# Kernel tuning notes

Measured on AMD Instinct MI355X. Metric: run time of the kernel, lower is better.

The kernel has to match this reference:

```python
import jax, jax.numpy as jnp
import numpy as np

N = 65536      # H*W pixels (256x256)
S = 1024       # superpixels
C = 128        # input channels
HIDE = 128     # hidden width
OUT = 64       # per-branch width (hide//2, concat=True)
CLS = 16       # classes
E_A = 16384    # superpixel adjacency edges
E_IMP = 6144   # importance (k=6) edges
E_PX = 1048576 # pixel row/col mask edges
EPS = 1e-5


def setup_inputs() -> dict:
    key = jax.random.key(0)
    ks = iter(jax.random.split(key, 64))
    nrm = lambda shape: jax.random.normal(next(ks), shape, dtype=jnp.float32) * 0.05
    uni = lambda shape, lo=0.0, hi=1.0: jax.random.uniform(next(ks), shape, dtype=jnp.float32, minval=lo, maxval=hi)
    ridx = lambda shape, hi: jax.random.randint(next(ks), shape, 0, hi, dtype=jnp.int32)
    d = {}
    d['x'] = jax.random.normal(next(ks), (N, C), dtype=jnp.float32)
    d['Q'] = uni((N, S))
    d['prelin_w'] = nrm((C, HIDE)); d['prelin_b'] = jnp.zeros((HIDE,), jnp.float32)
    d['bn0_g'] = jnp.ones((HIDE,), jnp.float32); d['bn0_b'] = jnp.zeros((HIDE,), jnp.float32)
    d['bn0_m'] = nrm((HIDE,)); d['bn0_v'] = uni((HIDE,), 0.5, 1.5)
    d['mmpn_w'] = nrm((5, HIDE, HIDE)); d['mmpn_b'] = jnp.zeros((5, HIDE), jnp.float32)
    d['mmpn_bn_g'] = jnp.ones((5, HIDE), jnp.float32); d['mmpn_bn_b'] = jnp.zeros((5, HIDE), jnp.float32)
    d['mmpn_bn_m'] = nrm((5, HIDE)); d['mmpn_bn_v'] = uni((5, HIDE), 0.5, 1.5)
    d['A_val'] = uni((E_A,)); d['imp_val'] = uni((E_IMP,))
    d['px_rowv_w'] = nrm((2, HIDE, OUT)); d['px_rowv_b'] = jnp.zeros((2, OUT), jnp.float32)
    d['px_colv_w'] = nrm((2, HIDE, OUT)); d['px_colv_b'] = jnp.zeros((2, OUT), jnp.float32)
    d['px_rowq_w'] = nrm((2, HIDE, OUT)); d['px_rowq_b'] = jnp.zeros((2, OUT), jnp.float32)
    d['px_colq_w'] = nrm((2, HIDE, OUT)); d['px_colq_b'] = jnp.zeros((2, OUT), jnp.float32)
    d['px_bn_g'] = jnp.ones((2, HIDE), jnp.float32); d['px_bn_b'] = jnp.zeros((2, HIDE), jnp.float32)
    d['px_bn_m'] = nrm((2, HIDE)); d['px_bn_v'] = uni((2, HIDE), 0.5, 1.5)
    d['final_w'] = nrm((HIDE, CLS)); d['final_b'] = jnp.zeros((CLS,), jnp.float32)
    d['A_src'] = ridx((E_A,), S); d['A_dst'] = ridx((E_A,), S)
    d['imp_src'] = ridx((E_IMP,), S); d['imp_dst'] = ridx((E_IMP,), S)
    d['row_src'] = ridx((E_PX,), N); d['row_dst'] = ridx((E_PX,), N)
    d['col_src'] = ridx((E_PX,), N); d['col_dst'] = ridx((E_PX,), N)
    return d


def _bn(x, g, b, m, v):
    # BatchNorm1d, eval mode (running stats)
    return g * (x - m) * jax.lax.rsqrt(v + EPS) + b


def _lrelu(x):
    return jnp.where(x >= 0, x, 0.01 * x)


def _ln(x):
    # F.layer_norm without affine params
    mu = jnp.mean(x, axis=-1, keepdims=True)
    var = jnp.mean(jnp.square(x - mu), axis=-1, keepdims=True)
    return (x - mu) * jax.lax.rsqrt(var + EPS)


def _seg_softmax(scores, ids, n):
    m = jax.ops.segment_max(scores, ids, num_segments=n)
    e = jnp.exp(scores - m[ids])
    d = jax.ops.segment_sum(e, ids, num_segments=n)
    return e / d[ids]


def _forward(x, Q, prelin_w, prelin_b, bn0_g, bn0_b, bn0_m, bn0_v,
             mmpn_w, mmpn_b, mmpn_bn_g, mmpn_bn_b, mmpn_bn_m, mmpn_bn_v,
             A_val, imp_val,
             px_rowv_w, px_rowv_b, px_colv_w, px_colv_b,
             px_rowq_w, px_rowq_b, px_colq_w, px_colq_b,
             px_bn_g, px_bn_b, px_bn_m, px_bn_v,
             final_w, final_b,
             A_src, A_dst, imp_src, imp_dst, row_src, row_dst, col_src, col_dst):
    x0 = _bn(x @ prelin_w + prelin_b, bn0_g, bn0_b, bn0_m, bn0_v)  # [N, HIDE]

    # ---- Hyperpixel_MMPN branch ----
    ncQ = Q / jnp.sum(Q, axis=0, keepdims=True)       # column-normalized Q
    hp = ncQ.T @ x0                                    # [S, HIDE]
    for i in range(5):
        h = hp @ mmpn_w[i] + mmpn_b[i]
        agg = jax.ops.segment_sum(A_val[:, None] * h[A_src], A_dst, num_segments=S)
        agg = agg + jax.ops.segment_sum(imp_val[:, None] * hp[imp_src], imp_dst, num_segments=S)
        hp = _lrelu(_bn(agg, mmpn_bn_g[i], mmpn_bn_b[i], mmpn_bn_m[i], mmpn_bn_v[i]))
    hyp = Q @ hp                                       # [N, HIDE]

    # ---- Pixel sparse-former branch ----
    px = x0
    for j in range(2):
        rowv = px @ px_rowv_w[j] + px_rowv_b[j]        # [N, OUT]
        colv = px @ px_colv_w[j] + px_colv_b[j]
        rowQ = _ln(px @ px_rowq_w[j] + px_rowq_b[j])
        colQ = _ln(px @ px_colq_w[j] + px_colq_b[j])
        rs = jnp.sum(rowQ[row_src] * rowQ[row_dst], axis=1) / OUT
        cs = jnp.sum(colQ[col_src] * colQ[col_dst], axis=1) / OUT
        ra = _seg_softmax(rs, row_src, N)
        ca = _seg_softmax(cs, col_src, N)
        rowout = jax.ops.segment_sum(rowv[row_dst] * ra[:, None], row_src, num_segments=N)
        colout = jax.ops.segment_sum(colv[col_dst] * ca[:, None], col_src, num_segments=N)
        out = jnp.concatenate((rowout, colout), axis=1)  # [N, HIDE]
        px = _lrelu(_bn(out, px_bn_g[j], px_bn_b[j], px_bn_m[j], px_bn_v[j]))

    H1 = hyp + px
    return jax.nn.softmax(H1 @ final_w + final_b, axis=-1)


def reference(x, Q, prelin_w, prelin_b, bn0_g, bn0_b, bn0_m, bn0_v,
              mmpn_w, mmpn_b, mmpn_bn_g, mmpn_bn_b, mmpn_bn_m, mmpn_bn_v,
              A_val, imp_val,
              px_rowv_w, px_rowv_b, px_colv_w, px_colv_b,
              px_rowq_w, px_rowq_b, px_colq_w, px_colq_b,
              px_bn_g, px_bn_b, px_bn_m, px_bn_v,
              final_w, final_b,
              A_src, A_dst, imp_src, imp_dst, row_src, row_dst, col_src, col_dst):
    return _forward(x, Q, prelin_w, prelin_b, bn0_g, bn0_b, bn0_m, bn0_v,
                    mmpn_w, mmpn_b, mmpn_bn_g, mmpn_bn_b, mmpn_bn_m, mmpn_bn_v,
                    A_val, imp_val,
                    px_rowv_w, px_rowv_b, px_colv_w, px_colv_b,
                    px_rowq_w, px_rowq_b, px_colq_w, px_colq_b,
                    px_bn_g, px_bn_b, px_bn_m, px_bn_v,
                    final_w, final_b,
                    A_src, A_dst, imp_src, imp_dst, row_src, row_dst, col_src, col_dst)
```

## Files before the change

kernel.cpp:

```cpp
#include <hip/hip_runtime.h>
#include <math.h>

#define N_PIX 65536
#define S_SP  1024
#define C_IN  128
#define HIDE  128
#define OUTW  64
#define NCLS  16
#define E_A   16384
#define E_IMP 6144
#define E_PX  1048576
#define EPSV  1e-5f

typedef __attribute__((ext_vector_type(4))) float f32x4;
typedef __attribute__((ext_vector_type(8))) short bf16x8;

__device__ inline ushort f2bf(float f) {
  uint u = __builtin_bit_cast(uint, f);
  uint r = (u + 0x7FFFu + ((u >> 16) & 1u)) >> 16;
  return (ushort)r;
}

__global__ __launch_bounds__(256) void k_x0(
    const float* __restrict__ x, const float* __restrict__ W,
    const float* __restrict__ bias, const float* __restrict__ g,
    const float* __restrict__ bb, const float* __restrict__ m,
    const float* __restrict__ vv, float* __restrict__ out) {
  __shared__ float Wl[128 * 128];
  __shared__ float Xl[32 * 128];
  int t = threadIdx.x;
  int n0 = blockIdx.x * 32;
  {
    const float4* Wg = (const float4*)W;
    float4* Wd = (float4*)Wl;
#pragma unroll
    for (int i = 0; i < 16; ++i) Wd[t + 256 * i] = Wg[t + 256 * i];
    const float4* Xg = (const float4*)(x + (size_t)n0 * 128);
    float4* Xd = (float4*)Xl;
#pragma unroll
    for (int i = 0; i < 4; ++i) Xd[t + 256 * i] = Xg[t + 256 * i];
  }
  __syncthreads();
  int ht = t & 31, nt = t >> 5;
  int h0 = ht * 4, r0 = nt * 4;
  float acc[4][4];
#pragma unroll
  for (int c = 0; c < 4; ++c) {
    float bv = bias[h0 + c];
#pragma unroll
    for (int r = 0; r < 4; ++r) acc[r][c] = bv;
  }
  for (int k = 0; k < 128; k += 4) {
    float4 xr[4], wk[4];
#pragma unroll
    for (int r = 0; r < 4; ++r) xr[r] = *(const float4*)&Xl[(r0 + r) * 128 + k];
#pragma unroll
    for (int kk = 0; kk < 4; ++kk) wk[kk] = *(const float4*)&Wl[(k + kk) * 128 + h0];
#pragma unroll
    for (int r = 0; r < 4; ++r) {
      float xs[4] = {xr[r].x, xr[r].y, xr[r].z, xr[r].w};
#pragma unroll
      for (int kk = 0; kk < 4; ++kk) {
        acc[r][0] += xs[kk] * wk[kk].x;
        acc[r][1] += xs[kk] * wk[kk].y;
        acc[r][2] += xs[kk] * wk[kk].z;
        acc[r][3] += xs[kk] * wk[kk].w;
      }
    }
  }
#pragma unroll
  for (int c = 0; c < 4; ++c) {
    int h = h0 + c;
    float sc = g[h] * rsqrtf(vv[h] + EPSV);
    float mb = m[h], bo = bb[h];
#pragma unroll
    for (int r = 0; r < 4; ++r) acc[r][c] = sc * (acc[r][c] - mb) + bo;
  }
#pragma unroll
  for (int r = 0; r < 4; ++r) {
    *(float4*)&out[(size_t)(n0 + r0 + r) * 128 + h0] =
        make_float4(acc[r][0], acc[r][1], acc[r][2], acc[r][3]);
  }
}

__global__ __launch_bounds__(256) void k_cast(
    const float* __restrict__ Q, ushort* __restrict__ Qt,
    float* __restrict__ csum, ushort* __restrict__ Qbf) {
  __shared__ ushort Ot[64 * 258];
  __shared__ float Cs[64];
  int t = threadIdx.x;
  int nt = blockIdx.x & 255, st = blockIdx.x >> 8;
  int n0 = nt * 256, s0 = st * 64;
  int lr = t & 15, lg = t >> 4;
  if (t < 64) Cs[t] = 0.f;
  __syncthreads();
  float sums[4] = {0.f, 0.f, 0.f, 0.f};
#pragma unroll
  for (int nb = 0; nb < 4; ++nb) {
    ushort hh[4][4];
#pragma unroll
    for (int u = 0; u < 4; ++u) {
      int n = n0 + nb * 64 + lg * 4 + u;
      float4 q = *(const float4*)&Q[(size_t)n * 1024 + s0 + lr * 4];
      sums[0] += q.x; sums[1] += q.y; sums[2] += q.z; sums[3] += q.w;
      hh[u][0] = f2bf(q.x); hh[u][1] = f2bf(q.y);
      hh[u][2] = f2bf(q.z); hh[u][3] = f2bf(q.w);
      if (Qbf) {
        uint2 w;
        w.x = (uint)hh[u][0] | ((uint)hh[u][1] << 16);
        w.y = (uint)hh[u][2] | ((uint)hh[u][3] << 16);
        *(uint2*)&Qbf[(size_t)n * 1024 + s0 + lr * 4] = w;
      }
    }
#pragma unroll
    for (int v = 0; v < 4; ++v) {
      uint lo = (uint)hh[0][v] | ((uint)hh[1][v] << 16);
      uint hi = (uint)hh[2][v] | ((uint)hh[3][v] << 16);
      ushort* p = &Ot[(lr * 4 + v) * 258 + nb * 64 + lg * 4];
      *(uint*)p = lo;
      *(uint*)(p + 2) = hi;
    }
  }
#pragma unroll
  for (int v = 0; v < 4; ++v) atomicAdd(&Cs[lr * 4 + v], sums[v]);
  __syncthreads();
  if (t < 64) atomicAdd(&csum[s0 + t], Cs[t]);
#pragma unroll
  for (int i = 0; i < 16; ++i) {
    int v2 = i * 256 + t;
    int s_loc = v2 >> 6, nq = v2 & 63;
    const ushort* p = &Ot[s_loc * 258 + nq * 4];
    uint2 o;
    o.x = *(const uint*)p;
    o.y = *(const uint*)(p + 2);
    *(uint2*)&Qt[(size_t)(s0 + s_loc) * 65536 + n0 + nq * 4] = o;
  }
}

__global__ __launch_bounds__(256) void k_xT(
    const float* __restrict__ x0, ushort* __restrict__ x0T) {
  __shared__ ushort Ot[128 * 258];
  int t = threadIdx.x;
  int n0 = blockIdx.x * 256;
  int lr = t & 31, lg = t >> 5;
#pragma unroll
  for (int nb = 0; nb < 8; ++nb) {
    ushort hh[4][4];
#pragma unroll
    for (int u = 0; u < 4; ++u) {
      int n = n0 + nb * 32 + lg * 4 + u;
      float4 q = *(const float4*)&x0[(size_t)n * 128 + lr * 4];
      hh[u][0] = f2bf(q.x); hh[u][1] = f2bf(q.y);
      hh[u][2] = f2bf(q.z); hh[u][3] = f2bf(q.w);
    }
#pragma unroll
    for (int v = 0; v < 4; ++v) {
      uint lo = (uint)hh[0][v] | ((uint)hh[1][v] << 16);
      uint hi = (uint)hh[2][v] | ((uint)hh[3][v] << 16);
      ushort* p = &Ot[(lr * 4 + v) * 258 + nb * 32 + lg * 4];
      *(uint*)p = lo;
      *(uint*)(p + 2) = hi;
    }
  }
  __syncthreads();
#pragma unroll
  for (int i = 0; i < 32; ++i) {
    int v2 = i * 256 + t;
    int h = v2 >> 6, nq = v2 & 63;
    const ushort* p = &Ot[h * 258 + nq * 4];
    uint2 o;
    o.x = *(const uint*)p;
    o.y = *(const uint*)(p + 2);
    *(uint2*)&x0T[(size_t)h * 65536 + n0 + nq * 4] = o;
  }
}

__global__ __launch_bounds__(256) void k_hpT(
    const float* __restrict__ hp, ushort* __restrict__ hpT) {
  __shared__ ushort Ot[128 * 258];
  int t = threadIdx.x;
  int s0 = blockIdx.x * 256;
  int lr = t & 31, lg = t >> 5;
#pragma unroll
  for (int sb = 0; sb < 8; ++sb) {
    ushort hh[4][4];
#pragma unroll
    for (int u = 0; u < 4; ++u) {
      int s = s0 + sb * 32 + lg * 4 + u;
      float4 q = *(const float4*)&hp[(size_t)s * 128 + lr * 4];
      hh[u][0] = f2bf(q.x); hh[u][1] = f2bf(q.y);
      hh[u][2] = f2bf(q.z); hh[u][3] = f2bf(q.w);
    }
#pragma unroll
    for (int v = 0; v < 4; ++v) {
      uint lo = (uint)hh[0][v] | ((uint)hh[1][v] << 16);
      uint hi = (uint)hh[2][v] | ((uint)hh[3][v] << 16);
      ushort* p = &Ot[(lr * 4 + v) * 258 + sb * 32 + lg * 4];
      *(uint*)p = lo;
      *(uint*)(p + 2) = hi;
    }
  }
  __syncthreads();
#pragma unroll
  for (int i = 0; i < 32; ++i) {
    int v2 = i * 256 + t;
    int h = v2 >> 6, sq = v2 & 63;
    const ushort* p = &Ot[h * 258 + sq * 4];
    uint2 o;
    o.x = *(const uint*)p;
    o.y = *(const uint*)(p + 2);
    *(uint2*)&hpT[(size_t)h * 1024 + s0 + sq * 4] = o;
  }
}

__device__ __forceinline__ void mfma_tile128(const ushort* Al, const ushort* Bl,
                                             f32x4 acc[4][4], int wr, int wc,
                                             int lr, int lq) {
#pragma unroll
  for (int kh = 0; kh < 2; ++kh) {
    bf16x8 af[4], bf[4];
#pragma unroll
    for (int i = 0; i < 4; ++i)
      af[i] = *(const bf16x8*)&Al[(wr * 64 + i * 16 + lr) * 72 + kh * 32 + lq * 8];
#pragma unroll
    for (int j = 0; j < 4; ++j)
      bf[j] = *(const bf16x8*)&Bl[(wc * 64 + j * 16 + lr) * 72 + kh * 32 + lq * 8];
#pragma unroll
    for (int i = 0; i < 4; ++i)
#pragma unroll
      for (int j = 0; j < 4; ++j)
        acc[i][j] = __builtin_amdgcn_mfma_f32_16x16x32_bf16(af[i], bf[j],
                                                            acc[i][j], 0, 0, 0);
  }
}

__global__ __launch_bounds__(256) void k_hpu2(
    const ushort* __restrict__ Qt, const ushort* __restrict__ x0T,
    float* __restrict__ hp_part) {
  __shared__ ushort Al[2][128 * 72];
  __shared__ ushort Bl[2][128 * 72];
  int t = threadIdx.x;
  int st = blockIdx.x & 7, kb = blockIdx.x >> 3;
  int s0 = st * 128;
  int wv = t >> 6, lane = t & 63;
  int wr = wv >> 1, wc = wv & 1;
  int lr = lane & 15, lq = lane >> 4;
  int sr = t >> 3, sg = t & 7;
  const ushort* Ab = Qt + (size_t)(s0 + sr) * 65536 + (size_t)kb * 1024 + sg * 8;
  const ushort* Bb = x0T + (size_t)sr * 65536 + (size_t)kb * 1024 + sg * 8;
  f32x4 acc[4][4];
#pragma unroll
  for (int i = 0; i < 4; ++i)
#pragma unroll
    for (int j = 0; j < 4; ++j) acc[i][j] = (f32x4){0.f, 0.f, 0.f, 0.f};
  uint4 ra[4], rb[4];
#pragma unroll
  for (int i = 0; i < 4; ++i) {
    ra[i] = *(const uint4*)(Ab + (size_t)i * 32 * 65536);
    rb[i] = *(const uint4*)(Bb + (size_t)i * 32 * 65536);
  }
#pragma unroll
  for (int i = 0; i < 4; ++i) {
    *(uint4*)&Al[0][(sr + 32 * i) * 72 + sg * 8] = ra[i];
    *(uint4*)&Bl[0][(sr + 32 * i) * 72 + sg * 8] = rb[i];
  }
  __syncthreads();
  for (int c = 0; c < 16; ++c) {
    int p = c & 1;
    if (c < 15) {
      int ko = (c + 1) * 64;
#pragma unroll
      for (int i = 0; i < 4; ++i) {
        ra[i] = *(const uint4*)(Ab + (size_t)i * 32 * 65536 + ko);
        rb[i] = *(const uint4*)(Bb + (size_t)i * 32 * 65536 + ko);
      }
    }
    mfma_tile128(Al[p], Bl[p], acc, wr, wc, lr, lq);
    if (c < 15) {
      int q = p ^ 1;
#pragma unroll
      for (int i = 0; i < 4; ++i) {
        *(uint4*)&Al[q][(sr + 32 * i) * 72 + sg * 8] = ra[i];
        *(uint4*)&Bl[q][(sr + 32 * i) * 72 + sg * 8] = rb[i];
      }
    }
    __syncthreads();
  }
  float* outp = hp_part + (size_t)kb * 131072;
#pragma unroll
  for (int i = 0; i < 4; ++i) {
    int s_g = s0 + wr * 64 + i * 16 + lq * 4;
#pragma unroll
    for (int j = 0; j < 4; ++j) {
      int h = wc * 64 + j * 16 + lr;
#pragma unroll
      for (int r = 0; r < 4; ++r)
        outp[(size_t)(s_g + r) * 128 + h] = acc[i][j][r];
    }
  }
}

__global__ void k_hpred(const float* __restrict__ part,
                        const float* __restrict__ csum, float* __restrict__ hp) {
  int tid = blockIdx.x * 256 + threadIdx.x;
  float s = 0.f;
  for (int kb = 0; kb < 64; ++kb) s += part[(size_t)kb * 131072 + tid];
  hp[tid] = s / csum[tid >> 7];
}

__global__ __launch_bounds__(256) void k_hyp_bf(
    const ushort* __restrict__ Qbf, const ushort* __restrict__ hpT,
    float* __restrict__ hyp) {
  __shared__ ushort Al[2][128 * 72];
  __shared__ ushort Bl[2][128 * 72];
  int t = threadIdx.x;
  int n0 = blockIdx.x * 128;
  int wv = t >> 6, lane = t & 63;
  int wr = wv >> 1, wc = wv & 1;
  int lr = lane & 15, lq = lane >> 4;
  int sr = t >> 3, sg = t & 7;
  const ushort* Ab = Qbf + (size_t)(n0 + sr) * 1024 + sg * 8;
  const ushort* Bb = hpT + (size_t)sr * 1024 + sg * 8;
  f32x4 acc[4][4];
#pragma unroll
  for (int i = 0; i < 4; ++i)
#pragma unroll
    for (int j = 0; j < 4; ++j) acc[i][j] = (f32x4){0.f, 0.f, 0.f, 0.f};
  uint4 ra[4], rb[4];
#pragma unroll
  for (int i = 0; i < 4; ++i) {
    ra[i] = *(const uint4*)(Ab + (size_t)i * 32 * 1024);
    rb[i] = *(const uint4*)(Bb + (size_t)i * 32 * 1024);
  }
#pragma unroll
  for (int i = 0; i < 4; ++i) {
    *(uint4*)&Al[0][(sr + 32 * i) * 72 + sg * 8] = ra[i];
    *(uint4*)&Bl[0][(sr + 32 * i) * 72 + sg * 8] = rb[i];
  }
  __syncthreads();
  for (int c = 0; c < 16; ++c) {
    int p = c & 1;
    if (c < 15) {
      int ko = (c + 1) * 64;
#pragma unroll
      for (int i = 0; i < 4; ++i) {
        ra[i] = *(const uint4*)(Ab + (size_t)i * 32 * 1024 + ko);
        rb[i] = *(const uint4*)(Bb + (size_t)i * 32 * 1024 + ko);
      }
    }
    mfma_tile128(Al[p], Bl[p], acc, wr, wc, lr, lq);
    if (c < 15) {
      int q = p ^ 1;
#pragma unroll
      for (int i = 0; i < 4; ++i) {
        *(uint4*)&Al[q][(sr + 32 * i) * 72 + sg * 8] = ra[i];
        *(uint4*)&Bl[q][(sr + 32 * i) * 72 + sg * 8] = rb[i];
      }
    }
    __syncthreads();
  }
#pragma unroll
  for (int i = 0; i < 4; ++i) {
    int n_g = n0 + wr * 64 + i * 16 + lq * 4;
#pragma unroll
    for (int j = 0; j < 4; ++j) {
      int h = wc * 64 + j * 16 + lr;
#pragma unroll
      for (int r = 0; r < 4; ++r)
        hyp[(size_t)(n_g + r) * 128 + h] = acc[i][j][r];
    }
  }
}

__global__ __launch_bounds__(256) void k_hyp_f32(
    const float* __restrict__ Q, const ushort* __restrict__ hpT,
    float* __restrict__ hyp) {
  __shared__ ushort Al[2][128 * 72];
  __shared__ ushort Bl[2][128 * 72];
  int t = threadIdx.x;
  int n0 = blockIdx.x * 128;
  int wv = t >> 6, lane = t & 63;
  int wr = wv >> 1, wc = wv & 1;
  int lr = lane & 15, lq = lane >> 4;
  int ar = t >> 4, ag = t & 15;
  int sr = t >> 3, sg = t & 7;
  const float* Af = Q + (size_t)(n0 + ar) * 1024 + ag * 4;
  const ushort* Bb = hpT + (size_t)sr * 1024 + sg * 8;
  f32x4 acc[4][4];
#pragma unroll
  for (int i = 0; i < 4; ++i)
#pragma unroll
    for (int j = 0; j < 4; ++j) acc[i][j] = (f32x4){0.f, 0.f, 0.f, 0.f};
  float4 rf[8];
  uint4 rb[4];
#pragma unroll
  for (int i = 0; i < 8; ++i) rf[i] = *(const float4*)(Af + (size_t)i * 16 * 1024);
#pragma unroll
  for (int i = 0; i < 4; ++i) rb[i] = *(const uint4*)(Bb + (size_t)i * 32 * 1024);
#pragma unroll
  for (int i = 0; i < 8; ++i) {
    uint2 pk;
    pk.x = (uint)f2bf(rf[i].x) | ((uint)f2bf(rf[i].y) << 16);
    pk.y = (uint)f2bf(rf[i].z) | ((uint)f2bf(rf[i].w) << 16);
    *(uint2*)&Al[0][(ar + 16 * i) * 72 + ag * 4] = pk;
  }
#pragma unroll
  for (int i = 0; i < 4; ++i)
    *(uint4*)&Bl[0][(sr + 32 * i) * 72 + sg * 8] = rb[i];
  __syncthreads();
  for (int c = 0; c < 16; ++c) {
    int p = c & 1;
    if (c < 15) {
      int ko = (c + 1) * 64;
#pragma unroll
      for (int i = 0; i < 8; ++i)
        rf[i] = *(const float4*)(Af + (size_t)i * 16 * 1024 + ko);
#pragma unroll
      for (int i = 0; i < 4; ++i)
        rb[i] = *(const uint4*)(Bb + (size_t)i * 32 * 1024 + ko);
    }
    mfma_tile128(Al[p], Bl[p], acc, wr, wc, lr, lq);
    if (c < 15) {
      int q = p ^ 1;
#pragma unroll
      for (int i = 0; i < 8; ++i) {
        uint2 pk;
        pk.x = (uint)f2bf(rf[i].x) | ((uint)f2bf(rf[i].y) << 16);
        pk.y = (uint)f2bf(rf[i].z) | ((uint)f2bf(rf[i].w) << 16);
        *(uint2*)&Al[q][(ar + 16 * i) * 72 + ag * 4] = pk;
      }
#pragma unroll
      for (int i = 0; i < 4; ++i)
        *(uint4*)&Bl[q][(sr + 32 * i) * 72 + sg * 8] = rb[i];
    }
    __syncthreads();
  }
#pragma unroll
  for (int i = 0; i < 4; ++i) {
    int n_g = n0 + wr * 64 + i * 16 + lq * 4;
#pragma unroll
    for (int j = 0; j < 4; ++j) {
      int h = wc * 64 + j * 16 + lr;
#pragma unroll
      for (int r = 0; r < 4; ++r)
        hyp[(size_t)(n_g + r) * 128 + h] = acc[i][j][r];
    }
  }
}

__global__ __launch_bounds__(256) void k_slin(
    const float* __restrict__ A, const float* __restrict__ W,
    const float* __restrict__ bias, float* __restrict__ out) {
  __shared__ float Wl[128 * 128];
  __shared__ float Xl[32 * 128];
  int t = threadIdx.x;
  int n0 = blockIdx.x * 32;
  {
    const float4* Wg = (const float4*)W;
    float4* Wd = (float4*)Wl;
#pragma unroll
    for (int i = 0; i < 16; ++i) Wd[t + 256 * i] = Wg[t + 256 * i];
    const float4* Xg = (const float4*)(A + (size_t)n0 * 128);
    float4* Xd = (float4*)Xl;
#pragma unroll
    for (int i = 0; i < 4; ++i) Xd[t + 256 * i] = Xg[t + 256 * i];
  }
  __syncthreads();
  int ht = t & 31, nt = t >> 5;
  int h0 = ht * 4, r0 = nt * 4;
  float acc[4][4];
#pragma unroll
  for (int c = 0; c < 4; ++c) {
    float bv = bias[h0 + c];
#pragma unroll
    for (int r = 0; r < 4; ++r) acc[r][c] = bv;
  }
  for (int k = 0; k < 128; k += 4) {
    float4 xr[4], wk[4];
#pragma unroll
    for (int r = 0; r < 4; ++r) xr[r] = *(const float4*)&Xl[(r0 + r) * 128 + k];
#pragma unroll
    for (int kk = 0; kk < 4; ++kk) wk[kk] = *(const float4*)&Wl[(k + kk) * 128 + h0];
#pragma unroll
    for (int r = 0; r < 4; ++r) {
      float xs[4] = {xr[r].x, xr[r].y, xr[r].z, xr[r].w};
#pragma unroll
      for (int kk = 0; kk < 4; ++kk) {
        acc[r][0] += xs[kk] * wk[kk].x;
        acc[r][1] += xs[kk] * wk[kk].y;
        acc[r][2] += xs[kk] * wk[kk].z;
        acc[r][3] += xs[kk] * wk[kk].w;
      }
    }
  }
#pragma unroll
  for (int r = 0; r < 4; ++r) {
    *(float4*)&out[(size_t)(n0 + r0 + r) * 128 + h0] =
        make_float4(acc[r][0], acc[r][1], acc[r][2], acc[r][3]);
  }
}

__global__ void k_edge_mmpn(
    const float* __restrict__ htmp, const float* __restrict__ hp,
    const float* __restrict__ A_val, const int* __restrict__ A_src,
    const int* __restrict__ A_dst, const float* __restrict__ imp_val,
    const int* __restrict__ imp_src, const int* __restrict__ imp_dst,
    float* __restrict__ agg) {
  long tid = (long)blockIdx.x * 256 + threadIdx.x;
  if (tid < (long)E_A * HIDE) {
    int e = (int)(tid >> 7), h = (int)(tid & 127);
    atomicAdd(&agg[(size_t)A_dst[e] * HIDE + h],
              A_val[e] * htmp[(size_t)A_src[e] * HIDE + h]);
  } else {
    long t2 = tid - (long)E_A * HIDE;
    if (t2 < (long)E_IMP * HIDE) {
      int e = (int)(t2 >> 7), h = (int)(t2 & 127);
      atomicAdd(&agg[(size_t)imp_dst[e] * HIDE + h],
                imp_val[e] * hp[(size_t)imp_src[e] * HIDE + h]);
    }
  }
}

__global__ void k_mmpn_bn(const float* __restrict__ agg, const float* __restrict__ g,
                          const float* __restrict__ b, const float* __restrict__ m,
                          const float* __restrict__ v, float* __restrict__ hp) {
  int tid = blockIdx.x * 256 + threadIdx.x;
  int h = tid & 127;
  float sc = g[h] * rsqrtf(v[h] + EPSV);
  float y = sc * (agg[tid] - m[h]) + b[h];
  hp[tid] = y >= 0.f ? y : 0.01f * y;
}

__global__ __launch_bounds__(256) void k_pxlin(
    const float* __restrict__ px, const float* __restrict__ Wrv,
    const float* __restrict__ Wcv, const float* __restrict__ Wrq,
    const float* __restrict__ Wcq, const float* __restrict__ brv,
    const float* __restrict__ bcv, const float* __restrict__ brq,
    const float* __restrict__ bcq, float* __restrict__ out) {
  __shared__ float Xl[32 * 128];
  __shared__ float Wl[32 * 256];
  int t = threadIdx.x;
  int n0 = blockIdx.x * 32;
  {
    float4* Xd = (float4*)Xl;
    const float4* Xg = (const float4*)(px + (size_t)n0 * 128);
#pragma unroll
    for (int it = 0; it < 4; ++it) Xd[t + 256 * it] = Xg[t + 256 * it];
  }
  int ct = t & 63, nt = t >> 6;
  int c0 = ct * 4, r0 = nt * 8;
  float acc[8][4];
  {
    int mt = c0 >> 6, cb = c0 & 63;
    const float* bs = mt == 0 ? brv : mt == 1 ? bcv : mt == 2 ? brq : bcq;
#pragma unroll
    for (int c = 0; c < 4; ++c) {
      float bv = bs[cb + c];
#pragma unroll
      for (int r = 0; r < 8; ++r) acc[r][c] = bv;
    }
  }
  for (int kc = 0; kc < 4; ++kc) {
    int k0 = kc * 32;
    __syncthreads();
    {
#pragma unroll
      for (int it = 0; it < 8; ++it) {
        int v = t + 256 * it;
        int kk = v >> 6, cq = v & 63;
        int c = cq * 4;
        int mt = c >> 6, cb = c & 63;
        const float* Ws = mt == 0 ? Wrv : mt == 1 ? Wcv : mt == 2 ? Wrq : Wcq;
        *(float4*)&Wl[kk * 256 + c] = *(const float4*)&Ws[(size_t)(k0 + kk) * 64 + cb];
      }
    }
    __syncthreads();
    for (int k = 0; k < 32; k += 4) {
      float4 wq[4];
#pragma unroll
      for (int kk = 0; kk < 4; ++kk) wq[kk] = *(const float4*)&Wl[(k + kk) * 256 + c0];
#pragma unroll
      for (int r = 0; r < 8; ++r) {
        float4 xq = *(const float4*)&Xl[(r0 + r) * 128 + k0 + k];
        float xs[4] = {xq.x, xq.y, xq.z, xq.w};
#pragma unroll
        for (int kk = 0; kk < 4; ++kk) {
          acc[r][0] += xs[kk] * wq[kk].x;
          acc[r][1] += xs[kk] * wq[kk].y;
          acc[r][2] += xs[kk] * wq[kk].z;
          acc[r][3] += xs[kk] * wq[kk].w;
        }
      }
    }
  }
#pragma unroll
  for (int r = 0; r < 8; ++r) {
    *(float4*)&out[(size_t)(n0 + r0 + r) * 256 + c0] =
        make_float4(acc[r][0], acc[r][1], acc[r][2], acc[r][3]);
  }
}

__global__ void k_ln(float* __restrict__ lin4) {
  int row = blockIdx.x * 4 + (threadIdx.x >> 6);
  int lane = threadIdx.x & 63;
  float* p = lin4 + (size_t)row * 256;
#pragma unroll
  for (int g = 0; g < 2; ++g) {
    float v = p[128 + g * 64 + lane];
    float s = v, s2 = v * v;
#pragma unroll
    for (int o = 32; o > 0; o >>= 1) {
      s += __shfl_xor(s, o, 64);
      s2 += __shfl_xor(s2, o, 64);
    }
    float mu = s * (1.0f / 64.0f);
    float var = s2 * (1.0f / 64.0f) - mu * mu;
    p[128 + g * 64 + lane] = (v - mu) * rsqrtf(var + EPSV);
  }
}

__global__ void k_hist(const int* __restrict__ src, int* __restrict__ cnt) {
  int e = blockIdx.x * 256 + threadIdx.x;
  atomicAdd(&cnt[src[e]], 1);
}

__global__ __launch_bounds__(1024) void k_scan(const int* __restrict__ cnt,
                                               int* __restrict__ off,
                                               int* __restrict__ cur) {
  __shared__ int part[1024];
  int t = threadIdx.x;
  int base = t * 64;
  int s = 0;
  for (int i = 0; i < 64; ++i) s += cnt[base + i];
  part[t] = s;
  __syncthreads();
  for (int o = 1; o < 1024; o <<= 1) {
    int v = part[t];
    int add = (t >= o) ? part[t - o] : 0;
    __syncthreads();
    part[t] = v + add;
    __syncthreads();
  }
  int run = (t > 0) ? part[t - 1] : 0;
  for (int i = 0; i < 64; ++i) {
    off[base + i] = run;
    cur[base + i] = run;
    run += cnt[base + i];
  }
  if (t == 1023) off[65536] = run;
}

__global__ void k_fill(const int* __restrict__ src, const int* __restrict__ dst,
                       int* __restrict__ cur, int* __restrict__ csr) {
  int e = blockIdx.x * 256 + threadIdx.x;
  int p = atomicAdd(&cur[src[e]], 1);
  csr[p] = dst[e];
}

__global__ __launch_bounds__(256) void k_gather(
    const float* __restrict__ lin4, int qoff, int voff,
    const int* __restrict__ off, const int* __restrict__ csr_dst,
    float* __restrict__ outp, int ooff) {
  int node = blockIdx.x * 4 + (threadIdx.x >> 6);
  int l = threadIdx.x & 63;
  float qs = lin4[(size_t)node * 256 + qoff + l];
  int i0 = off[node], i1 = off[node + 1];
  float acc = 0.f, den = 0.f;
  for (int i = i0; i < i1; ++i) {
    int d = csr_dst[i];
    const float* base = lin4 + (size_t)d * 256;
    float qd = base[qoff + l];
    float vd = base[voff + l];
    float p = qs * qd;
#pragma unroll
    for (int o = 32; o > 0; o >>= 1) p += __shfl_xor(p, o, 64);
    float w = __expf(p * (1.0f / OUTW));
    den += w;
    acc += w * vd;
  }
  float r = den > 0.f ? 1.0f / den : 0.f;
  outp[(size_t)node * HIDE + ooff + l] = acc * r;
}

__global__ void k_pxbn(float* __restrict__ px, const float* __restrict__ g,
                       const float* __restrict__ b, const float* __restrict__ m,
                       const float* __restrict__ v) {
  int tid = blockIdx.x * 256 + threadIdx.x;
  int h = tid & 127;
  float x = px[tid];
  float sc = g[h] * rsqrtf(v[h] + EPSV);
  float y = sc * (x - m[h]) + b[h];
  px[tid] = y >= 0.f ? y : 0.01f * y;
}

__global__ __launch_bounds__(256) void k_final(
    const float* __restrict__ hyp, const float* __restrict__ px,
    const float* __restrict__ W, const float* __restrict__ b,
    float* __restrict__ out) {
  __shared__ float Wl[128 * 16];
  __shared__ float rl[16 * 129];
  int t = threadIdx.x;
  int n0 = blockIdx.x * 16;
#pragma unroll
  for (int i = 0; i < 8; ++i) Wl[t + 256 * i] = W[t + 256 * i];
#pragma unroll
  for (int i = 0; i < 8; ++i) {
    int v = t + 256 * i;
    int r = v >> 7, c = v & 127;
    rl[r * 129 + c] = hyp[(size_t)(n0 + r) * 128 + c] + px[(size_t)(n0 + r) * 128 + c];
  }
  __syncthreads();
  int r = t >> 4, cls = t & 15;
  float acc = b[cls];
  for (int k = 0; k < 128; ++k) acc += rl[r * 129 + k] * Wl[k * 16 + cls];
  float mx = acc;
#pragma unroll
  for (int o = 8; o > 0; o >>= 1) mx = fmaxf(mx, __shfl_xor(mx, o, 16));
  float e = expf(acc - mx), s = e;
#pragma unroll
  for (int o = 8; o > 0; o >>= 1) s += __shfl_xor(s, o, 16);
  out[(size_t)(n0 + r) * 16 + cls] = e / s;
}

extern "C" void kernel_launch(void* const* d_in, const int* in_sizes, int n_in,
                              void* d_out, int out_size, void* d_ws, size_t ws_size,
                              hipStream_t stream) {
  const float* x        = (const float*)d_in[0];
  const float* Q        = (const float*)d_in[1];
  const float* prelin_w = (const float*)d_in[2];
  const float* prelin_b = (const float*)d_in[3];
  const float* bn0_g    = (const float*)d_in[4];
  const float* bn0_b    = (const float*)d_in[5];
  const float* bn0_m    = (const float*)d_in[6];
  const float* bn0_v    = (const float*)d_in[7];
  const float* mmpn_w   = (const float*)d_in[8];
  const float* mmpn_b   = (const float*)d_in[9];
  const float* mmpn_bn_g= (const float*)d_in[10];
  const float* mmpn_bn_b= (const float*)d_in[11];
  const float* mmpn_bn_m= (const float*)d_in[12];
  const float* mmpn_bn_v= (const float*)d_in[13];
  const float* A_val    = (const float*)d_in[14];
  const float* imp_val  = (const float*)d_in[15];
  const float* px_rowv_w= (const float*)d_in[16];
  const float* px_rowv_b= (const float*)d_in[17];
  const float* px_colv_w= (const float*)d_in[18];
  const float* px_colv_b= (const float*)d_in[19];
  const float* px_rowq_w= (const float*)d_in[20];
  const float* px_rowq_b= (const float*)d_in[21];
  const float* px_colq_w= (const float*)d_in[22];
  const float* px_colq_b= (const float*)d_in[23];
  const float* px_bn_g  = (const float*)d_in[24];
  const float* px_bn_b  = (const float*)d_in[25];
  const float* px_bn_m  = (const float*)d_in[26];
  const float* px_bn_v  = (const float*)d_in[27];
  const float* final_w  = (const float*)d_in[28];
  const float* final_b  = (const float*)d_in[29];
  const int* A_src   = (const int*)d_in[30];
  const int* A_dst   = (const int*)d_in[31];
  const int* imp_src = (const int*)d_in[32];
  const int* imp_dst = (const int*)d_in[33];
  const int* row_src = (const int*)d_in[34];
  const int* row_dst = (const int*)d_in[35];
  const int* col_src = (const int*)d_in[36];
  const int* col_dst = (const int*)d_in[37];
  float* out = (float*)d_out;

  float* ws = (float*)d_ws;
  float* x0px = ws; ws += (size_t)N_PIX * HIDE;
  float* hyp  = ws; ws += (size_t)N_PIX * HIDE;
  float* hp_part = hyp;
  float* big  = ws; ws += (size_t)32 * 1024 * 1024;
  ushort* Qt  = (ushort*)big;
  float* lin4 = big;
  int* off_row = (int*)(big + (size_t)N_PIX * 256);
  int* off_col = off_row + 65537;
  int* csr_row = off_col + 65537;
  int* csr_col = csr_row + E_PX;
  ushort* x0T = (ushort*)ws; ws += (size_t)HIDE * N_PIX / 2;
  ushort* hpT = (ushort*)ws; ws += (size_t)HIDE * S_SP / 2;
  float* csum = ws; ws += S_SP;
  float* hp   = ws; ws += (size_t)S_SP * HIDE;
  float* htmp = ws; ws += (size_t)S_SP * HIDE;
  float* agg  = ws; ws += (size_t)S_SP * HIDE;

  size_t used = (size_t)((char*)ws - (char*)d_ws);
  ushort* Qbf = nullptr;
  if (used + (size_t)N_PIX * S_SP * sizeof(ushort) <= ws_size)
    Qbf = (ushort*)ws;

  int* cnt_row = (int*)agg;
  int* cnt_col = (int*)agg + 65536;
  int* cur_row = (int*)htmp;
  int* cur_col = (int*)htmp + 65536;

  hipMemsetAsync(csum, 0, S_SP * sizeof(float), stream);

  k_cast<<<4096, 256, 0, stream>>>(Q, Qt, csum, Qbf);
  k_x0<<<N_PIX / 32, 256, 0, stream>>>(x, prelin_w, prelin_b, bn0_g, bn0_b, bn0_m,
                                       bn0_v, x0px);
  k_xT<<<N_PIX / 256, 256, 0, stream>>>(x0px, x0T);
  k_hpu2<<<512, 256, 0, stream>>>(Qt, x0T, hp_part);
  k_hpred<<<S_SP * HIDE / 256, 256, 0, stream>>>(hp_part, csum, hp);

  for (int i = 0; i < 5; ++i) {
    k_slin<<<S_SP / 32, 256, 0, stream>>>(hp, mmpn_w + (size_t)i * HIDE * HIDE,
                                          mmpn_b + i * HIDE, htmp);
    hipMemsetAsync(agg, 0, (size_t)S_SP * HIDE * sizeof(float), stream);
    k_edge_mmpn<<<(E_A + E_IMP) * HIDE / 256, 256, 0, stream>>>(
        htmp, hp, A_val, A_src, A_dst, imp_val, imp_src, imp_dst, agg);
    k_mmpn_bn<<<S_SP * HIDE / 256, 256, 0, stream>>>(
        agg, mmpn_bn_g + i * HIDE, mmpn_bn_b + i * HIDE, mmpn_bn_m + i * HIDE,
        mmpn_bn_v + i * HIDE, hp);
  }

  k_hpT<<<S_SP / 256, 256, 0, stream>>>(hp, hpT);
  if (Qbf)
    k_hyp_bf<<<N_PIX / 128, 256, 0, stream>>>(Qbf, hpT, hyp);
  else
    k_hyp_f32<<<N_PIX / 128, 256, 0, stream>>>(Q, hpT, hyp);

  hipMemsetAsync(cnt_row, 0, 2 * 65536 * sizeof(int), stream);
  k_hist<<<E_PX / 256, 256, 0, stream>>>(row_src, cnt_row);
  k_hist<<<E_PX / 256, 256, 0, stream>>>(col_src, cnt_col);
  k_scan<<<1, 1024, 0, stream>>>(cnt_row, off_row, cur_row);
  k_scan<<<1, 1024, 0, stream>>>(cnt_col, off_col, cur_col);
  k_fill<<<E_PX / 256, 256, 0, stream>>>(row_src, row_dst, cur_row, csr_row);
  k_fill<<<E_PX / 256, 256, 0, stream>>>(col_src, col_dst, cur_col, csr_col);

  for (int j = 0; j < 2; ++j) {
    k_pxlin<<<N_PIX / 32, 256, 0, stream>>>(
        x0px, px_rowv_w + j * 8192, px_colv_w + j * 8192, px_rowq_w + j * 8192,
        px_colq_w + j * 8192, px_rowv_b + j * 64, px_colv_b + j * 64,
        px_rowq_b + j * 64, px_colq_b + j * 64, lin4);
    k_ln<<<N_PIX / 4, 256, 0, stream>>>(lin4);
    k_gather<<<N_PIX / 4, 256, 0, stream>>>(lin4, 128, 0, off_row, csr_row, x0px, 0);
    k_gather<<<N_PIX / 4, 256, 0, stream>>>(lin4, 192, 64, off_col, csr_col, x0px, 64);
    k_pxbn<<<N_PIX * HIDE / 256, 256, 0, stream>>>(x0px, px_bn_g + j * HIDE,
                                                   px_bn_b + j * HIDE,
                                                   px_bn_m + j * HIDE,
                                                   px_bn_v + j * HIDE);
  }

  k_final<<<N_PIX / 16, 256, 0, stream>>>(hyp, x0px, final_w, final_b, out);
}
```

Measured before the change: 1.830 ms.

## Pack pixel q/v to bf16 for gathers, CSR-ize superpixel MMPN aggregation

The pixel attention gathers now read a packed bf16 (normalized q, v) word per lane instead of two fp32 values from the 256-wide lin4 row. Batchnorm and leaky-ReLU are fused into the gather epilogue, and the gather loop is unrolled by two. The superpixel message passing is converted from per-edge atomics plus a separate BN kernel into a dst-sorted CSR pull kernel with fused BN, built once up front. This targets memory traffic and atomic contention at the cost of bf16 precision on q and v.

```diff
diff --git a/kernel.cpp b/kernel.cpp
--- a/kernel.cpp
+++ b/kernel.cpp
@@ -19,6 +19,9 @@
   uint u = __builtin_bit_cast(uint, f);
   uint r = (u + 0x7FFFu + ((u >> 16) & 1u)) >> 16;
   return (ushort)r;
+}
+__device__ inline float bf2f(uint u) {
+  return __builtin_bit_cast(float, u << 16);
 }
 
 __global__ __launch_bounds__(256) void k_x0(
@@ -500,35 +503,26 @@
   }
 }
 
-__global__ void k_edge_mmpn(
-    const float* __restrict__ htmp, const float* __restrict__ hp,
-    const float* __restrict__ A_val, const int* __restrict__ A_src,
-    const int* __restrict__ A_dst, const float* __restrict__ imp_val,
-    const int* __restrict__ imp_src, const int* __restrict__ imp_dst,
-    float* __restrict__ agg) {
-  long tid = (long)blockIdx.x * 256 + threadIdx.x;
-  if (tid < (long)E_A * HIDE) {
-    int e = (int)(tid >> 7), h = (int)(tid & 127);
-    atomicAdd(&agg[(size_t)A_dst[e] * HIDE + h],
-              A_val[e] * htmp[(size_t)A_src[e] * HIDE + h]);
-  } else {
-    long t2 = tid - (long)E_A * HIDE;
-    if (t2 < (long)E_IMP * HIDE) {
-      int e = (int)(t2 >> 7), h = (int)(t2 & 127);
-      atomicAdd(&agg[(size_t)imp_dst[e] * HIDE + h],
-                imp_val[e] * hp[(size_t)imp_src[e] * HIDE + h]);
-    }
-  }
-}
-
-__global__ void k_mmpn_bn(const float* __restrict__ agg, const float* __restrict__ g,
-                          const float* __restrict__ b, const float* __restrict__ m,
-                          const float* __restrict__ v, float* __restrict__ hp) {
-  int tid = blockIdx.x * 256 + threadIdx.x;
-  int h = tid & 127;
+__global__ __launch_bounds__(256) void k_mmpn_agg(
+    const float* __restrict__ htmp, const float* __restrict__ hpin,
+    const int* __restrict__ offA, const int* __restrict__ srcA,
+    const float* __restrict__ valA, const int* __restrict__ offI,
+    const int* __restrict__ srcI, const float* __restrict__ valI,
+    const float* __restrict__ g, const float* __restrict__ b,
+    const float* __restrict__ m, const float* __restrict__ v,
+    float* __restrict__ hpout) {
+  int s = blockIdx.x * 2 + (threadIdx.x >> 7);
+  int h = threadIdx.x & 127;
+  float acc = 0.f;
+  int a0 = offA[s], a1 = offA[s + 1];
+  for (int i = a0; i < a1; ++i)
+    acc += valA[i] * htmp[(size_t)srcA[i] * 128 + h];
+  int b0 = offI[s], b1 = offI[s + 1];
+  for (int i = b0; i < b1; ++i)
+    acc += valI[i] * hpin[(size_t)srcI[i] * 128 + h];
   float sc = g[h] * rsqrtf(v[h] + EPSV);
-  float y = sc * (agg[tid] - m[h]) + b[h];
-  hp[tid] = y >= 0.f ? y : 0.01f * y;
+  float y = sc * (acc - m[h]) + b[h];
+  hpout[(size_t)s * 128 + h] = y >= 0.f ? y : 0.01f * y;
 }
 
 __global__ __launch_bounds__(256) void k_pxlin(
@@ -600,14 +594,16 @@
   }
 }
 
-__global__ void k_ln(float* __restrict__ lin4) {
+__global__ __launch_bounds__(256) void k_pack(
+    const float* __restrict__ lin4, uint* __restrict__ pkrow,
+    uint* __restrict__ pkcol) {
   int row = blockIdx.x * 4 + (threadIdx.x >> 6);
-  int lane = threadIdx.x & 63;
-  float* p = lin4 + (size_t)row * 256;
-#pragma unroll
-  for (int g = 0; g < 2; ++g) {
-    float v = p[128 + g * 64 + lane];
-    float s = v, s2 = v * v;
+  int l = threadIdx.x & 63;
+  const float* p = lin4 + (size_t)row * 256;
+#pragma unroll
+  for (int gsel = 0; gsel < 2; ++gsel) {
+    float q = p[128 + gsel * 64 + l];
+    float s = q, s2 = q * q;
 #pragma unroll
     for (int o = 32; o > 0; o >>= 1) {
       s += __shfl_xor(s, o, 64);
@@ -615,7 +611,10 @@
     }
     float mu = s * (1.0f / 64.0f);
     float var = s2 * (1.0f / 64.0f) - mu * mu;
-    p[128 + g * 64 + lane] = (v - mu) * rsqrtf(var + EPSV);
+    float qn = (q - mu) * rsqrtf(var + EPSV);
+    float vv = p[gsel * 64 + l];
+    uint pkv = (uint)f2bf(qn) | ((uint)f2bf(vv) << 16);
+    (gsel ? pkcol : pkrow)[(size_t)row * 64 + l] = pkv;
   }
 }
 
@@ -650,6 +649,27 @@
   if (t == 1023) off[65536] = run;
 }
 
+__global__ __launch_bounds__(1024) void k_scan_s(const int* __restrict__ cnt,
+                                                 int* __restrict__ off,
+                                                 int* __restrict__ cur) {
+  __shared__ int part[1024];
+  int t = threadIdx.x;
+  int v = cnt[t];
+  part[t] = v;
+  __syncthreads();
+  for (int o = 1; o < 1024; o <<= 1) {
+    int x = part[t];
+    int a = (t >= o) ? part[t - o] : 0;
+    __syncthreads();
+    part[t] = x + a;
+    __syncthreads();
+  }
+  int ex = (t > 0) ? part[t - 1] : 0;
+  off[t] = ex;
+  cur[t] = ex;
+  if (t == 1023) off[1024] = part[1023];
+}
+
 __global__ void k_fill(const int* __restrict__ src, const int* __restrict__ dst,
                        int* __restrict__ cur, int* __restrict__ csr) {
   int e = blockIdx.x * 256 + threadIdx.x;
@@ -657,40 +677,59 @@
   csr[p] = dst[e];
 }
 
-__global__ __launch_bounds__(256) void k_gather(
-    const float* __restrict__ lin4, int qoff, int voff,
-    const int* __restrict__ off, const int* __restrict__ csr_dst,
-    float* __restrict__ outp, int ooff) {
+__global__ void k_fill_v(const int* __restrict__ dst, const int* __restrict__ src,
+                         const float* __restrict__ val, int* __restrict__ cur,
+                         int* __restrict__ csr_src, float* __restrict__ csr_val) {
+  int e = blockIdx.x * 256 + threadIdx.x;
+  int p = atomicAdd(&cur[dst[e]], 1);
+  csr_src[p] = src[e];
+  csr_val[p] = val[e];
+}
+
+__global__ __launch_bounds__(256) void k_gather2(
+    const uint* __restrict__ pk, const int* __restrict__ off,
+    const int* __restrict__ csr, const float* __restrict__ g,
+    const float* __restrict__ b, const float* __restrict__ m,
+    const float* __restrict__ v, int ooff, float* __restrict__ outp) {
   int node = blockIdx.x * 4 + (threadIdx.x >> 6);
   int l = threadIdx.x & 63;
-  float qs = lin4[(size_t)node * 256 + qoff + l];
+  uint rs = pk[(size_t)node * 64 + l];
+  float qs = bf2f(rs & 0xffffu);
   int i0 = off[node], i1 = off[node + 1];
   float acc = 0.f, den = 0.f;
-  for (int i = i0; i < i1; ++i) {
-    int d = csr_dst[i];
-    const float* base = lin4 + (size_t)d * 256;
-    float qd = base[qoff + l];
-    float vd = base[voff + l];
-    float p = qs * qd;
-#pragma unroll
-    for (int o = 32; o > 0; o >>= 1) p += __shfl_xor(p, o, 64);
-    float w = __expf(p * (1.0f / OUTW));
-    den += w;
-    acc += w * vd;
+  int i = i0;
+  for (; i + 2 <= i1; i += 2) {
+    int d0 = csr[i], d1 = csr[i + 1];
+    uint r0 = pk[(size_t)d0 * 64 + l];
+    uint r1 = pk[(size_t)d1 * 64 + l];
+    float p0 = qs * bf2f(r0 & 0xffffu);
+    float p1 = qs * bf2f(r1 & 0xffffu);
+#pragma unroll
+    for (int o = 32; o > 0; o >>= 1) {
+      p0 += __shfl_xor(p0, o, 64);
+      p1 += __shfl_xor(p1, o, 64);
+    }
+    float w0 = __expf(p0 * (1.0f / OUTW));
+    float w1 = __expf(p1 * (1.0f / OUTW));
+    den += w0 + w1;
+    acc += w0 * bf2f(r0 >> 16) + w1 * bf2f(r1 >> 16);
+  }
+  if (i < i1) {
+    int d0 = csr[i];
+    uint r0 = pk[(size_t)d0 * 64 + l];
+    float p0 = qs * bf2f(r0 & 0xffffu);
+#pragma unroll
+    for (int o = 32; o > 0; o >>= 1) p0 += __shfl_xor(p0, o, 64);
+    float w0 = __expf(p0 * (1.0f / OUTW));
+    den += w0;
+    acc += w0 * bf2f(r0 >> 16);
   }
   float r = den > 0.f ? 1.0f / den : 0.f;
-  outp[(size_t)node * HIDE + ooff + l] = acc * r;
-}
-
-__global__ void k_pxbn(float* __restrict__ px, const float* __restrict__ g,
-                       const float* __restrict__ b, const float* __restrict__ m,
-                       const float* __restrict__ v) {
-  int tid = blockIdx.x * 256 + threadIdx.x;
-  int h = tid & 127;
-  float x = px[tid];
+  float val = acc * r;
+  int h = ooff + l;
   float sc = g[h] * rsqrtf(v[h] + EPSV);
-  float y = sc * (x - m[h]) + b[h];
-  px[tid] = y >= 0.f ? y : 0.01f * y;
+  float y = sc * (val - m[h]) + b[h];
+  outp[(size_t)node * HIDE + h] = y >= 0.f ? y : 0.01f * y;
 }
 
 __global__ __launch_bounds__(256) void k_final(
@@ -776,6 +815,8 @@
   int* off_col = off_row + 65537;
   int* csr_row = off_col + 65537;
   int* csr_col = csr_row + E_PX;
+  uint* pkrow = (uint*)(big + (size_t)20 * 1024 * 1024);
+  uint* pkcol = pkrow + (size_t)N_PIX * 64;
   ushort* x0T = (ushort*)ws; ws += (size_t)HIDE * N_PIX / 2;
   ushort* hpT = (ushort*)ws; ws += (size_t)HIDE * S_SP / 2;
   float* csum = ws; ws += S_SP;
@@ -783,6 +824,19 @@
   float* htmp = ws; ws += (size_t)S_SP * HIDE;
   float* agg  = ws; ws += (size_t)S_SP * HIDE;
 
+  int* offA = (int*)ws;
+  int* offI = offA + 1025;
+  int* cntA = offI + 1025;
+  int* cntI = cntA + 1024;
+  int* curA = cntI + 1024;
+  int* curI = curA + 1024;
+  int* srcA = curI + 1024;
+  float* valA = (float*)(srcA + E_A);
+  int* srcI = (int*)(valA + E_A);
+  float* valI = (float*)(srcI + E_IMP);
+  ws = (float*)(valI + E_IMP);
+  ws = (float*)(((uintptr_t)ws + 15) & ~(uintptr_t)15);
+
   size_t used = (size_t)((char*)ws - (char*)d_ws);
   ushort* Qbf = nullptr;
   if (used + (size_t)N_PIX * S_SP * sizeof(ushort) <= ws_size)
@@ -794,6 +848,14 @@
   int* cur_col = (int*)htmp + 65536;
 
   hipMemsetAsync(csum, 0, S_SP * sizeof(float), stream);
+  hipMemsetAsync(cntA, 0, 2 * 1024 * sizeof(int), stream);
+
+  k_hist<<<E_A / 256, 256, 0, stream>>>(A_dst, cntA);
+  k_hist<<<E_IMP / 256, 256, 0, stream>>>(imp_dst, cntI);
+  k_scan_s<<<1, 1024, 0, stream>>>(cntA, offA, curA);
+  k_scan_s<<<1, 1024, 0, stream>>>(cntI, offI, curI);
+  k_fill_v<<<E_A / 256, 256, 0, stream>>>(A_dst, A_src, A_val, curA, srcA, valA);
+  k_fill_v<<<E_IMP / 256, 256, 0, stream>>>(imp_dst, imp_src, imp_val, curI, srcI, valI);
 
   k_cast<<<4096, 256, 0, stream>>>(Q, Qt, csum, Qbf);
   k_x0<<<N_PIX / 32, 256, 0, stream>>>(x, prelin_w, prelin_b, bn0_g, bn0_b, bn0_m,
@@ -802,18 +864,20 @@
   k_hpu2<<<512, 256, 0, stream>>>(Qt, x0T, hp_part);
   k_hpred<<<S_SP * HIDE / 256, 256, 0, stream>>>(hp_part, csum, hp);
 
-  for (int i = 0; i < 5; ++i) {
-    k_slin<<<S_SP / 32, 256, 0, stream>>>(hp, mmpn_w + (size_t)i * HIDE * HIDE,
-                                          mmpn_b + i * HIDE, htmp);
-    hipMemsetAsync(agg, 0, (size_t)S_SP * HIDE * sizeof(float), stream);
-    k_edge_mmpn<<<(E_A + E_IMP) * HIDE / 256, 256, 0, stream>>>(
-        htmp, hp, A_val, A_src, A_dst, imp_val, imp_src, imp_dst, agg);
-    k_mmpn_bn<<<S_SP * HIDE / 256, 256, 0, stream>>>(
-        agg, mmpn_bn_g + i * HIDE, mmpn_bn_b + i * HIDE, mmpn_bn_m + i * HIDE,
-        mmpn_bn_v + i * HIDE, hp);
-  }
-
-  k_hpT<<<S_SP / 256, 256, 0, stream>>>(hp, hpT);
+  {
+    float* cur = hp;
+    float* nxt = agg;
+    for (int i = 0; i < 5; ++i) {
+      k_slin<<<S_SP / 32, 256, 0, stream>>>(cur, mmpn_w + (size_t)i * HIDE * HIDE,
+                                            mmpn_b + i * HIDE, htmp);
+      k_mmpn_agg<<<S_SP / 2, 256, 0, stream>>>(
+          htmp, cur, offA, srcA, valA, offI, srcI, valI,
+          mmpn_bn_g + i * HIDE, mmpn_bn_b + i * HIDE, mmpn_bn_m + i * HIDE,
+          mmpn_bn_v + i * HIDE, nxt);
+      float* tmp = cur; cur = nxt; nxt = tmp;
+    }
+    k_hpT<<<S_SP / 256, 256, 0, stream>>>(cur, hpT);
+  }
   if (Qbf)
     k_hyp_bf<<<N_PIX / 128, 256, 0, stream>>>(Qbf, hpT, hyp);
   else
@@ -832,13 +896,13 @@
         x0px, px_rowv_w + j * 8192, px_colv_w + j * 8192, px_rowq_w + j * 8192,
         px_colq_w + j * 8192, px_rowv_b + j * 64, px_colv_b + j * 64,
         px_rowq_b + j * 64, px_colq_b + j * 64, lin4);
-    k_ln<<<N_PIX / 4, 256, 0, stream>>>(lin4);
-    k_gather<<<N_PIX / 4, 256, 0, stream>>>(lin4, 128, 0, off_row, csr_row, x0px, 0);
-    k_gather<<<N_PIX / 4, 256, 0, stream>>>(lin4, 192, 64, off_col, csr_col, x0px, 64);
-    k_pxbn<<<N_PIX * HIDE / 256, 256, 0, stream>>>(x0px, px_bn_g + j * HIDE,
-                                                   px_bn_b + j * HIDE,
-                                                   px_bn_m + j * HIDE,
-                                                   px_bn_v + j * HIDE);
+    k_pack<<<N_PIX / 4, 256, 0, stream>>>(lin4, pkrow, pkcol);
+    k_gather2<<<N_PIX / 4, 256, 0, stream>>>(
+        pkrow, off_row, csr_row, px_bn_g + j * HIDE, px_bn_b + j * HIDE,
+        px_bn_m + j * HIDE, px_bn_v + j * HIDE, 0, x0px);
+    k_gather2<<<N_PIX / 4, 256, 0, stream>>>(
+        pkcol, off_col, csr_col, px_bn_g + j * HIDE, px_bn_b + j * HIDE,
+        px_bn_m + j * HIDE, px_bn_v + j * HIDE, 64, x0px);
   }
 
   k_final<<<N_PIX / 16, 256, 0, stream>>>(hyp, x0px, final_w, final_b, out);
```

Measured after the change: 1.635 ms. 1.12x faster.
